# Optimization experiments

Hardware: AMD Instinct MI355X
Metric: run time of the kernel (lower is better)

Reference implementation:

```python
import jax, jax.numpy as jnp
import numpy as np

N = 100000   # num nodes
E = 1600000  # num edges (avg degree 16)
D = 32       # input_dim == latent_size
L = 3        # num_layers
K = 3        # num_hops


def setup_inputs() -> dict:
    key = jax.random.key(0)
    k0, k1, k2, k3, k4 = jax.random.split(key, 5)
    x = jax.random.normal(k0, (N, D), dtype=jnp.float32)
    edge_index = jax.random.randint(k1, (2, E), 0, N, dtype=jnp.int32)
    edge_weight = jax.random.uniform(k2, (E,), dtype=jnp.float32)
    # TAGConv per layer: K+1 bias-free Linear(in,out) weights + one bias
    W = jax.random.normal(k3, (L, K + 1, D, D), dtype=jnp.float32) * (1.0 / np.sqrt(D))
    b = jax.random.normal(k4, (L, D), dtype=jnp.float32) * 0.01
    return {"x": x, "edge_index": edge_index, "edge_weight": edge_weight, "W": W, "b": b}


def reference(x, edge_index, edge_weight, W, b):
    row, col = edge_index[0], edge_index[1]  # source, target
    # PyG gcn_norm with add_self_loops=False: deg at target, symmetric norm
    deg = jax.ops.segment_sum(edge_weight, col, num_segments=N)
    safe = jnp.where(deg > 0, deg, 1.0)
    dis = jnp.where(deg > 0, jax.lax.rsqrt(safe), 0.0)  # deg^{-1/2}
    norm = dis[row] * edge_weight * dis[col]            # [E]
    for l in range(L):
        out = x @ W[l, 0]
        h = x
        for k in range(1, K + 1):
            # one hop of normalized sparse aggregation: out[col] += norm * h[row]
            h = jax.ops.segment_sum(h[row] * norm[:, None], col, num_segments=N)
            out = out + h @ W[l, k]
        x = jax.nn.relu(out + b[l])
    return x
```

## Files before the change

### kernel.cpp

```cpp
#include <hip/hip_runtime.h>
#include <hip/hip_fp16.h>

#define NN 100000
#define NE 1600000
#define DD 32
#define NL 3
#define NK 3

#define BK 512
#define NBK ((NN + BK - 1) / BK)
#define EA 4096
#define GA ((NE + EA - 1) / EA)
#define NCNT (NBK * GA)
#define NSC ((NCNT + 255) / 256)
#define CB (NN * DD / 4 / 256)

typedef _Float16 half8 __attribute__((ext_vector_type(8)));
typedef float f32x4 __attribute__((ext_vector_type(4)));

__global__ void countA_kernel(const int* __restrict__ col, unsigned* __restrict__ cntAB,
                              const float* __restrict__ x, __half* __restrict__ xh,
                              const float* __restrict__ W, half8* __restrict__ Bpk) {
    __shared__ unsigned hc[NBK];
    int bid = blockIdx.x;
    int t = threadIdx.x;
    if (bid < GA) {
        for (int i = t; i < NBK; i += 256) hc[i] = 0;
        __syncthreads();
        int e0 = bid * EA;
        int e1 = e0 + EA; if (e1 > NE) e1 = NE;
        for (int e = e0 + t; e < e1; e += 256)
            atomicAdd(&hc[((unsigned)col[e]) >> 9], 1u);
        __syncthreads();
        for (int i = t; i < NBK; i += 256)
            cntAB[i * GA + bid] = hc[i];
    } else if (bid < GA + CB) {
        int i = (bid - GA) * 256 + t;
        f32x4 v = ((const f32x4*)x)[i];
        __half2 h01 = __floats2half2_rn(v.x, v.y);
        __half2 h23 = __floats2half2_rn(v.z, v.w);
        int2 o;
        o.x = *(int*)&h01; o.y = *(int*)&h23;
        ((int2*)xh)[i] = o;
    } else if (t < 64) {
        int l = bid - GA - CB;
        int m = t & 15, kq = t >> 4;
        for (int c = 0; c < 4; ++c) {
            for (int h = 0; h < 2; ++h) {
                half8 hi, lo;
                for (int j = 0; j < 8; ++j) {
                    float wv = W[(size_t)((l * 4 + c) * DD + kq * 8 + j) * DD + h * 16 + m];
                    _Float16 wh = (_Float16)wv;
                    hi[j] = wh;
                    lo[j] = (_Float16)(wv - (float)wh);
                }
                Bpk[(size_t)(((l * 4 + c) * 2 + h) * 2 + 0) * 64 + t] = hi;
                Bpk[(size_t)(((l * 4 + c) * 2 + h) * 2 + 1) * 64 + t] = lo;
            }
        }
    }
}

__global__ void scanb_kernel(unsigned* __restrict__ a, unsigned* __restrict__ bsum) {
    __shared__ unsigned s[256];
    int t = threadIdx.x;
    int i = blockIdx.x * 256 + t;
    unsigned v = (i < NCNT) ? a[i] : 0u;
    s[t] = v;
    __syncthreads();
    for (int off = 1; off < 256; off <<= 1) {
        unsigned add = (t >= off) ? s[t - off] : 0u;
        __syncthreads();
        s[t] += add;
        __syncthreads();
    }
    if (i < NCNT) a[i] = s[t] - v;
    if (t == 255) bsum[blockIdx.x] = s[255];
}

__global__ void scant_kernel(unsigned* __restrict__ bsum) {
    __shared__ unsigned s[512];
    int t = threadIdx.x;
    unsigned v = (t < NSC) ? bsum[t] : 0u;
    s[t] = v;
    __syncthreads();
    for (int off = 1; off < 512; off <<= 1) {
        unsigned add = (t >= off) ? s[t - off] : 0u;
        __syncthreads();
        s[t] += add;
        __syncthreads();
    }
    if (t < NSC) bsum[t] = s[t] - v;
}

__global__ void scana_kernel(unsigned* __restrict__ a, const unsigned* __restrict__ bsum,
                             unsigned* __restrict__ bbase) {
    int i = blockIdx.x * 256 + threadIdx.x;
    if (i < NCNT) {
        unsigned v = a[i] + bsum[i >> 8];
        a[i] = v;
        if (i % GA == 0) bbase[i / GA] = v;
    }
    if (i == 0) bbase[NBK] = NE;
}

__global__ void scatterC_kernel(const int* __restrict__ row, const int* __restrict__ col,
                                const float* __restrict__ w,
                                const unsigned* __restrict__ cntAB, int2* __restrict__ eb) {
    __shared__ unsigned cur[NBK];
    int bid = blockIdx.x;
    int t = threadIdx.x;
    for (int i = t; i < NBK; i += 256) cur[i] = cntAB[i * GA + bid];
    __syncthreads();
    int e0 = bid * EA;
    int e1 = e0 + EA; if (e1 > NE) e1 = NE;
    for (int e = e0 + t; e < e1; e += 256) {
        unsigned c = (unsigned)col[e];
        unsigned pos = atomicAdd(&cur[c >> 9], 1u);
        eb[pos] = make_int2((int)(((c & 511u) << 17) | (unsigned)row[e]),
                            __float_as_int(w[e]));
    }
}

__global__ void histD1_kernel(const int2* __restrict__ eb, const unsigned* __restrict__ bbase,
                              int* __restrict__ ptr, float* __restrict__ dis) {
    __shared__ unsigned h[BK];
    __shared__ unsigned ps[256];
    int b = blockIdx.x;
    int t = threadIdx.x;
    h[t] = 0; h[t + 256] = 0;
    __syncthreads();
    unsigned e0 = bbase[b], e1 = bbase[b + 1];
    for (unsigned e = e0 + t; e < e1; e += 256) {
        int2 E = eb[e];
        unsigned cl = ((unsigned)E.x) >> 17;
        float wv = __int_as_float(E.y);
        atomicAdd(&h[cl], (1u << 24) | (unsigned)(wv * 131072.0f));
    }
    __syncthreads();
    unsigned c0 = h[2 * t] >> 24, c1 = h[2 * t + 1] >> 24;
    unsigned pv = c0 + c1;
    ps[t] = pv;
    __syncthreads();
    for (int off = 1; off < 256; off <<= 1) {
        unsigned add = (t >= off) ? ps[t - off] : 0u;
        __syncthreads();
        ps[t] += add;
        __syncthreads();
    }
    unsigned base = e0 + ps[t] - pv;
    int n0 = b * BK + 2 * t;
    if (n0 < NN) {
        ptr[n0] = (int)base;
        float dg = (float)(h[2 * t] & 0xFFFFFFu) * (1.0f / 131072.0f);
        dis[n0] = dg > 0.f ? rsqrtf(dg) : 0.f;
    }
    if (n0 + 1 < NN) {
        ptr[n0 + 1] = (int)(base + c0);
        float dg = (float)(h[2 * t + 1] & 0xFFFFFFu) * (1.0f / 131072.0f);
        dis[n0 + 1] = dg > 0.f ? rsqrtf(dg) : 0.f;
    }
    if (b == 0 && t == 0) ptr[NN] = NE;
}

__global__ void fillD2_kernel(const int2* __restrict__ eb, const unsigned* __restrict__ bbase,
                              const int* __restrict__ ptr, const float* __restrict__ dis,
                              unsigned* __restrict__ epair) {
    __shared__ unsigned cur[BK];
    __shared__ float dl[BK];
    int b = blockIdx.x;
    int t = threadIdx.x;
    int n0 = b * BK;
    for (int i = t; i < BK; i += 256) {
        int n = n0 + i;
        cur[i] = (n < NN) ? (unsigned)ptr[n] : 0u;
        dl[i] = (n < NN) ? dis[n] : 0.f;
    }
    __syncthreads();
    unsigned e0 = bbase[b], e1 = bbase[b + 1];
    for (unsigned e = e0 + t; e < e1; e += 256) {
        int2 E = eb[e];
        unsigned cl = ((unsigned)E.x) >> 17;
        unsigned r = ((unsigned)E.x) & 0x1FFFFu;
        float nv = dis[r] * __int_as_float(E.y) * dl[cl];
        unsigned pos = atomicAdd(&cur[cl], 1u);
        unsigned hb = (unsigned)__half_as_ushort(__float2half(nv));
        epair[pos] = (hb << 17) | r;
    }
}

#define ACC8(rw, vv)                                                             \
    {                                                                            \
        float2 f0 = __half22float2(*reinterpret_cast<__half2*>(&rw.x));          \
        float2 f1 = __half22float2(*reinterpret_cast<__half2*>(&rw.y));          \
        float2 f2 = __half22float2(*reinterpret_cast<__half2*>(&rw.z));          \
        float2 f3 = __half22float2(*reinterpret_cast<__half2*>(&rw.w));          \
        agg[0] = fmaf(vv, f0.x, agg[0]); agg[1] = fmaf(vv, f0.y, agg[1]);        \
        agg[2] = fmaf(vv, f1.x, agg[2]); agg[3] = fmaf(vv, f1.y, agg[3]);        \
        agg[4] = fmaf(vv, f2.x, agg[4]); agg[5] = fmaf(vv, f2.y, agg[5]);        \
        agg[6] = fmaf(vv, f3.x, agg[6]); agg[7] = fmaf(vv, f3.y, agg[7]);        \
    }

__device__ __forceinline__ void gather_body16(const ushort* __restrict__ hin,
                                              const unsigned* __restrict__ epair,
                                              int p0, int p1, int st, int c4,
                                              float agg[8]) {
    const int4* hin4 = (const int4*)hin;
    int e = p0 + st;
    if (e < p1) {
        unsigned pw[8];
        int4 rw[8];
        #pragma unroll
        for (int d = 0; d < 8; ++d) {
            int ed = e + 4 * d;
            pw[d] = epair[ed < p1 ? ed : p1 - 1];
        }
        #pragma unroll
        for (int d = 0; d < 8; ++d)
            rw[d] = hin4[(size_t)(pw[d] & 0x1FFFFu) * 4 + c4];
        #pragma unroll
        for (int d = 0; d < 8; ++d) {
            float vv = (e + 4 * d < p1)
                ? __half2float(__ushort_as_half((unsigned short)(pw[d] >> 17))) : 0.f;
            ACC8(rw[d], vv);
        }
        for (e = p0 + st + 32; e < p1; e += 4) {
            unsigned p = epair[e];
            int4 r = hin4[(size_t)(p & 0x1FFFFu) * 4 + c4];
            float vv = __half2float(__ushort_as_half((unsigned short)(p >> 17)));
            ACC8(r, vv);
        }
    }
    #pragma unroll
    for (int i = 0; i < 8; ++i) {
        agg[i] += __shfl_xor(agg[i], 4, 16);
        agg[i] += __shfl_xor(agg[i], 8, 16);
    }
}

__global__ __launch_bounds__(256) void gather_kernel(
    const ushort* __restrict__ hin, ushort* __restrict__ hout,
    const int* __restrict__ ptr, const unsigned* __restrict__ epair) {
    int tid = threadIdx.x;
    int lane16 = tid & 15;
    int st = lane16 >> 2, c4 = lane16 & 3;
    int n = blockIdx.x * 16 + (tid >> 4);
    int p0 = ptr[n], p1 = ptr[n + 1];
    float agg[8] = {0.f, 0.f, 0.f, 0.f, 0.f, 0.f, 0.f, 0.f};
    gather_body16(hin, epair, p0, p1, st, c4, agg);
    if (lane16 < 4) {
        __half2 ha = __floats2half2_rn(agg[0], agg[1]);
        __half2 hb = __floats2half2_rn(agg[2], agg[3]);
        __half2 hc = __floats2half2_rn(agg[4], agg[5]);
        __half2 hd = __floats2half2_rn(agg[6], agg[7]);
        int4 pkv;
        pkv.x = *(int*)&ha; pkv.y = *(int*)&hb;
        pkv.z = *(int*)&hc; pkv.w = *(int*)&hd;
        ((int4*)hout)[(size_t)n * 4 + lane16] = pkv;
    }
}

__global__ __launch_bounds__(256) void k3ep_kernel(
    const ushort* __restrict__ f0, const ushort* __restrict__ h1,
    const ushort* __restrict__ h2,
    ushort* __restrict__ f0out, float* __restrict__ outf,
    const int* __restrict__ ptr, const unsigned* __restrict__ epair,
    const half8* __restrict__ Bp, const float* __restrict__ bias, int last) {
    __shared__ __half ldsH[16 * DD];
    int tid = threadIdx.x;
    int lane16 = tid & 15;
    int st = lane16 >> 2, c4 = lane16 & 3;
    int nloc = tid >> 4;
    int n0 = blockIdx.x * 16;
    int n = n0 + nloc;
    int p0 = ptr[n], p1 = ptr[n + 1];
    float agg[8] = {0.f, 0.f, 0.f, 0.f, 0.f, 0.f, 0.f, 0.f};
    gather_body16(h2, epair, p0, p1, st, c4, agg);
    if (lane16 < 4) {
        __half2 ha = __floats2half2_rn(agg[0], agg[1]);
        __half2 hb = __floats2half2_rn(agg[2], agg[3]);
        __half2 hc = __floats2half2_rn(agg[4], agg[5]);
        __half2 hd = __floats2half2_rn(agg[6], agg[7]);
        int4 pkv;
        pkv.x = *(int*)&ha; pkv.y = *(int*)&hb;
        pkv.z = *(int*)&hc; pkv.w = *(int*)&hd;
        *(int4*)&ldsH[nloc * DD + lane16 * 8] = pkv;
    }
    __syncthreads();
    if (tid < 64) {
        int m = tid & 15, kq = tid >> 4;
        int ai = (n0 + m) * 4 + kq;
        const half8* A0 = (const half8*)f0;
        const half8* A1 = (const half8*)h1;
        const half8* A2 = (const half8*)h2;
        f32x4 acc0 = {0.f, 0.f, 0.f, 0.f};
        f32x4 acc1 = {0.f, 0.f, 0.f, 0.f};
        half8 a;
        a = A0[ai];
        acc0 = __builtin_amdgcn_mfma_f32_16x16x32_f16(a, Bp[0 * 64 + tid], acc0, 0, 0, 0);
        acc0 = __builtin_amdgcn_mfma_f32_16x16x32_f16(a, Bp[1 * 64 + tid], acc0, 0, 0, 0);
        acc1 = __builtin_amdgcn_mfma_f32_16x16x32_f16(a, Bp[2 * 64 + tid], acc1, 0, 0, 0);
        acc1 = __builtin_amdgcn_mfma_f32_16x16x32_f16(a, Bp[3 * 64 + tid], acc1, 0, 0, 0);
        a = A1[ai];
        acc0 = __builtin_amdgcn_mfma_f32_16x16x32_f16(a, Bp[4 * 64 + tid], acc0, 0, 0, 0);
        acc0 = __builtin_amdgcn_mfma_f32_16x16x32_f16(a, Bp[5 * 64 + tid], acc0, 0, 0, 0);
        acc1 = __builtin_amdgcn_mfma_f32_16x16x32_f16(a, Bp[6 * 64 + tid], acc1, 0, 0, 0);
        acc1 = __builtin_amdgcn_mfma_f32_16x16x32_f16(a, Bp[7 * 64 + tid], acc1, 0, 0, 0);
        a = A2[ai];
        acc0 = __builtin_amdgcn_mfma_f32_16x16x32_f16(a, Bp[8 * 64 + tid], acc0, 0, 0, 0);
        acc0 = __builtin_amdgcn_mfma_f32_16x16x32_f16(a, Bp[9 * 64 + tid], acc0, 0, 0, 0);
        acc1 = __builtin_amdgcn_mfma_f32_16x16x32_f16(a, Bp[10 * 64 + tid], acc1, 0, 0, 0);
        acc1 = __builtin_amdgcn_mfma_f32_16x16x32_f16(a, Bp[11 * 64 + tid], acc1, 0, 0, 0);
        a = *(const half8*)&ldsH[m * DD + kq * 8];
        acc0 = __builtin_amdgcn_mfma_f32_16x16x32_f16(a, Bp[12 * 64 + tid], acc0, 0, 0, 0);
        acc0 = __builtin_amdgcn_mfma_f32_16x16x32_f16(a, Bp[13 * 64 + tid], acc0, 0, 0, 0);
        acc1 = __builtin_amdgcn_mfma_f32_16x16x32_f16(a, Bp[14 * 64 + tid], acc1, 0, 0, 0);
        acc1 = __builtin_amdgcn_mfma_f32_16x16x32_f16(a, Bp[15 * 64 + tid], acc1, 0, 0, 0);
        float b0 = bias[m], b1 = bias[16 + m];
        #pragma unroll
        for (int r = 0; r < 4; ++r) {
            int rowi = n0 + kq * 4 + r;
            float v0 = fmaxf(acc0[r] + b0, 0.f);
            float v1 = fmaxf(acc1[r] + b1, 0.f);
            if (last) {
                outf[rowi * DD + m] = v0;
                outf[rowi * DD + 16 + m] = v1;
            } else {
                ((__half*)f0out)[rowi * DD + m] = __float2half(v0);
                ((__half*)f0out)[rowi * DD + 16 + m] = __float2half(v1);
            }
        }
    }
}

extern "C" void kernel_launch(void* const* d_in, const int* in_sizes, int n_in,
                              void* d_out, int out_size, void* d_ws, size_t ws_size,
                              hipStream_t stream) {
    const float* x  = (const float*)d_in[0];
    const int*   ei = (const int*)d_in[1];
    const float* ew = (const float*)d_in[2];
    const float* W  = (const float*)d_in[3];
    const float* b  = (const float*)d_in[4];
    float* out = (float*)d_out;

    const int* row = ei;
    const int* col = ei + NE;

    char* base = (char*)d_ws;
    int2*     eb    = (int2*)base;
    ushort*   h1    = (ushort*)base;
    ushort*   h2    = (ushort*)(base + 6400000);
    unsigned* epair = (unsigned*)(base + 12800000);
    ushort*   f0    = (ushort*)(base + 19200000);
    int*      ptr   = (int*)(base + 25600000);
    float*    dis   = (float*)(base + 26000016);
    unsigned* cntAB = (unsigned*)(base + 26400016);
    unsigned* bsum  = (unsigned*)(base + 26706560);
    unsigned* bbase = (unsigned*)(base + 26707776);
    half8*    Bpk   = (half8*)(base + 26708576);

    countA_kernel<<<GA + CB + NL, 256, 0, stream>>>(col, cntAB, x, (__half*)f0, W, Bpk);
    scanb_kernel<<<NSC, 256, 0, stream>>>(cntAB, bsum);
    scant_kernel<<<1, 512, 0, stream>>>(bsum);
    scana_kernel<<<NSC, 256, 0, stream>>>(cntAB, bsum, bbase);
    scatterC_kernel<<<GA, 256, 0, stream>>>(row, col, ew, cntAB, eb);
    histD1_kernel<<<NBK, 256, 0, stream>>>(eb, bbase, ptr, dis);
    fillD2_kernel<<<NBK, 256, 0, stream>>>(eb, bbase, ptr, dis, epair);

    const int grid = NN / 16;
    for (int l = 0; l < NL; ++l) {
        int lastl = (l == NL - 1);
        gather_kernel<<<grid, 256, 0, stream>>>(f0, h1, ptr, epair);
        gather_kernel<<<grid, 256, 0, stream>>>(h1, h2, ptr, epair);
        k3ep_kernel<<<grid, 256, 0, stream>>>(f0, h1, h2, f0, out, ptr, epair,
                                              Bpk + (size_t)l * 1024,
                                              b + (size_t)l * DD, lastl);
    }
}
```

Before: 315.0 us.

## Split feature matrices into lo/hi column planes and use persistent gather grids

Node features are stored as two 16-column half planes instead of one 32-column row, and each gather pass processes one plane at a time. The likely aim is to halve the working set per pass so random neighbor reads hit cache more often. The gather and fused epilogue kernels become persistent grid-stride loops over 1024 blocks with occupancy hints, and edge-list loads and stores are marked nontemporal. In exchange, epair and ptr are read twice per hop, and the fused kernel keeps several tiles in LDS with a per-tile barrier.

Result: slower. 442.7 us (+40.5%).

```diff
diff --git a/kernel.cpp b/kernel.cpp
--- a/kernel.cpp
+++ b/kernel.cpp
@@ -15,11 +15,17 @@
 #define NSC ((NCNT + 255) / 256)
 #define CB (NN * DD / 4 / 256)
 
+#define GRID 1024
+#define NG (NN / 16)
+#define GMAX 7
+
 typedef _Float16 half8 __attribute__((ext_vector_type(8)));
 typedef float f32x4 __attribute__((ext_vector_type(4)));
+typedef int i32x4 __attribute__((ext_vector_type(4)));
 
 __global__ void countA_kernel(const int* __restrict__ col, unsigned* __restrict__ cntAB,
-                              const float* __restrict__ x, __half* __restrict__ xh,
+                              const float* __restrict__ x,
+                              __half* __restrict__ xlo, __half* __restrict__ xhi,
                               const float* __restrict__ W, half8* __restrict__ Bpk) {
     __shared__ unsigned hc[NBK];
     int bid = blockIdx.x;
@@ -41,7 +47,9 @@
         __half2 h23 = __floats2half2_rn(v.z, v.w);
         int2 o;
         o.x = *(int*)&h01; o.y = *(int*)&h23;
-        ((int2*)xh)[i] = o;
+        int n = i >> 3, j = i & 7;
+        __half* dst = (j < 4) ? xlo : xhi;
+        ((int2*)dst)[n * 4 + (j & 3)] = o;
     } else if (t < 64) {
         int l = bid - GA - CB;
         int m = t & 15, kq = t >> 4;
@@ -201,133 +209,174 @@
         agg[6] = fmaf(vv, f3.x, agg[6]); agg[7] = fmaf(vv, f3.y, agg[7]);        \
     }
 
-__device__ __forceinline__ void gather_body16(const ushort* __restrict__ hin,
-                                              const unsigned* __restrict__ epair,
-                                              int p0, int p1, int st, int c4,
-                                              float agg[8]) {
-    const int4* hin4 = (const int4*)hin;
+__device__ __forceinline__ void gseg(const ushort* __restrict__ pin,
+                                     const unsigned* __restrict__ epair,
+                                     int p0, int p1, int st, int c2,
+                                     float agg[8]) {
+    const int4* pin4 = (const int4*)pin;
     int e = p0 + st;
     if (e < p1) {
-        unsigned pw[8];
-        int4 rw[8];
+        unsigned pw[4];
+        int4 rw[4];
         #pragma unroll
-        for (int d = 0; d < 8; ++d) {
-            int ed = e + 4 * d;
-            pw[d] = epair[ed < p1 ? ed : p1 - 1];
+        for (int d = 0; d < 4; ++d) {
+            int ed = e + 8 * d;
+            pw[d] = __builtin_nontemporal_load(epair + (ed < p1 ? ed : p1 - 1));
         }
         #pragma unroll
-        for (int d = 0; d < 8; ++d)
-            rw[d] = hin4[(size_t)(pw[d] & 0x1FFFFu) * 4 + c4];
+        for (int d = 0; d < 4; ++d)
+            rw[d] = pin4[(size_t)(pw[d] & 0x1FFFFu) * 2 + c2];
         #pragma unroll
-        for (int d = 0; d < 8; ++d) {
-            float vv = (e + 4 * d < p1)
+        for (int d = 0; d < 4; ++d) {
+            float vv = (e + 8 * d < p1)
                 ? __half2float(__ushort_as_half((unsigned short)(pw[d] >> 17))) : 0.f;
             ACC8(rw[d], vv);
         }
-        for (e = p0 + st + 32; e < p1; e += 4) {
-            unsigned p = epair[e];
-            int4 r = hin4[(size_t)(p & 0x1FFFFu) * 4 + c4];
+        for (e = p0 + st + 32; e < p1; e += 8) {
+            unsigned p = __builtin_nontemporal_load(epair + e);
+            int4 r = pin4[(size_t)(p & 0x1FFFFu) * 2 + c2];
             float vv = __half2float(__ushort_as_half((unsigned short)(p >> 17)));
             ACC8(r, vv);
         }
     }
     #pragma unroll
     for (int i = 0; i < 8; ++i) {
+        agg[i] += __shfl_xor(agg[i], 2, 16);
         agg[i] += __shfl_xor(agg[i], 4, 16);
         agg[i] += __shfl_xor(agg[i], 8, 16);
     }
 }
 
-__global__ __launch_bounds__(256) void gather_kernel(
-    const ushort* __restrict__ hin, ushort* __restrict__ hout,
+__device__ __forceinline__ void hop_plane(const ushort* __restrict__ pin,
+                                          ushort* __restrict__ pout,
+                                          const int* __restrict__ ptr,
+                                          const unsigned* __restrict__ epair,
+                                          int tid, int bid) {
+    int lane16 = tid & 15;
+    int st = lane16 >> 1, c2 = lane16 & 1;
+    int nl = tid >> 4;
+    for (int g = bid; g < NG; g += GRID) {
+        int n = g * 16 + nl;
+        int p0 = ptr[n], p1 = ptr[n + 1];
+        float agg[8] = {0.f, 0.f, 0.f, 0.f, 0.f, 0.f, 0.f, 0.f};
+        gseg(pin, epair, p0, p1, st, c2, agg);
+        if (lane16 < 2) {
+            __half2 ha = __floats2half2_rn(agg[0], agg[1]);
+            __half2 hb = __floats2half2_rn(agg[2], agg[3]);
+            __half2 hc = __floats2half2_rn(agg[4], agg[5]);
+            __half2 hd = __floats2half2_rn(agg[6], agg[7]);
+            i32x4 pkv;
+            pkv[0] = *(int*)&ha; pkv[1] = *(int*)&hb;
+            pkv[2] = *(int*)&hc; pkv[3] = *(int*)&hd;
+            __builtin_nontemporal_store(pkv, (i32x4*)pout + (size_t)n * 2 + c2);
+        }
+    }
+}
+
+__global__ __launch_bounds__(256, 4) void gather_kernel(
+    const ushort* __restrict__ pin_lo, const ushort* __restrict__ pin_hi,
+    ushort* __restrict__ pout_lo, ushort* __restrict__ pout_hi,
     const int* __restrict__ ptr, const unsigned* __restrict__ epair) {
     int tid = threadIdx.x;
-    int lane16 = tid & 15;
-    int st = lane16 >> 2, c4 = lane16 & 3;
-    int n = blockIdx.x * 16 + (tid >> 4);
-    int p0 = ptr[n], p1 = ptr[n + 1];
-    float agg[8] = {0.f, 0.f, 0.f, 0.f, 0.f, 0.f, 0.f, 0.f};
-    gather_body16(hin, epair, p0, p1, st, c4, agg);
-    if (lane16 < 4) {
-        __half2 ha = __floats2half2_rn(agg[0], agg[1]);
-        __half2 hb = __floats2half2_rn(agg[2], agg[3]);
-        __half2 hc = __floats2half2_rn(agg[4], agg[5]);
-        __half2 hd = __floats2half2_rn(agg[6], agg[7]);
-        int4 pkv;
-        pkv.x = *(int*)&ha; pkv.y = *(int*)&hb;
-        pkv.z = *(int*)&hc; pkv.w = *(int*)&hd;
-        ((int4*)hout)[(size_t)n * 4 + lane16] = pkv;
-    }
-}
-
-__global__ __launch_bounds__(256) void k3ep_kernel(
-    const ushort* __restrict__ f0, const ushort* __restrict__ h1,
-    const ushort* __restrict__ h2,
-    ushort* __restrict__ f0out, float* __restrict__ outf,
+    int bid = blockIdx.x;
+    hop_plane(pin_lo, pout_lo, ptr, epair, tid, bid);
+    hop_plane(pin_hi, pout_hi, ptr, epair, tid, bid);
+}
+
+__global__ __launch_bounds__(256, 4) void k3ep_kernel(
+    const ushort* __restrict__ f0lo, const ushort* __restrict__ f0hi,
+    const ushort* __restrict__ h1lo, const ushort* __restrict__ h1hi,
+    const ushort* __restrict__ h2lo, const ushort* __restrict__ h2hi,
+    ushort* __restrict__ f0outlo, ushort* __restrict__ f0outhi,
+    float* __restrict__ outf,
     const int* __restrict__ ptr, const unsigned* __restrict__ epair,
     const half8* __restrict__ Bp, const float* __restrict__ bias, int last) {
-    __shared__ __half ldsH[16 * DD];
+    __shared__ __align__(16) __half ldsT[GMAX][16 * DD];
     int tid = threadIdx.x;
+    int bid = blockIdx.x;
     int lane16 = tid & 15;
-    int st = lane16 >> 2, c4 = lane16 & 3;
-    int nloc = tid >> 4;
-    int n0 = blockIdx.x * 16;
-    int n = n0 + nloc;
-    int p0 = ptr[n], p1 = ptr[n + 1];
-    float agg[8] = {0.f, 0.f, 0.f, 0.f, 0.f, 0.f, 0.f, 0.f};
-    gather_body16(h2, epair, p0, p1, st, c4, agg);
-    if (lane16 < 4) {
-        __half2 ha = __floats2half2_rn(agg[0], agg[1]);
-        __half2 hb = __floats2half2_rn(agg[2], agg[3]);
-        __half2 hc = __floats2half2_rn(agg[4], agg[5]);
-        __half2 hd = __floats2half2_rn(agg[6], agg[7]);
-        int4 pkv;
-        pkv.x = *(int*)&ha; pkv.y = *(int*)&hb;
-        pkv.z = *(int*)&hc; pkv.w = *(int*)&hd;
-        *(int4*)&ldsH[nloc * DD + lane16 * 8] = pkv;
-    }
-    __syncthreads();
-    if (tid < 64) {
-        int m = tid & 15, kq = tid >> 4;
-        int ai = (n0 + m) * 4 + kq;
-        const half8* A0 = (const half8*)f0;
-        const half8* A1 = (const half8*)h1;
-        const half8* A2 = (const half8*)h2;
-        f32x4 acc0 = {0.f, 0.f, 0.f, 0.f};
-        f32x4 acc1 = {0.f, 0.f, 0.f, 0.f};
-        half8 a;
-        a = A0[ai];
-        acc0 = __builtin_amdgcn_mfma_f32_16x16x32_f16(a, Bp[0 * 64 + tid], acc0, 0, 0, 0);
-        acc0 = __builtin_amdgcn_mfma_f32_16x16x32_f16(a, Bp[1 * 64 + tid], acc0, 0, 0, 0);
-        acc1 = __builtin_amdgcn_mfma_f32_16x16x32_f16(a, Bp[2 * 64 + tid], acc1, 0, 0, 0);
-        acc1 = __builtin_amdgcn_mfma_f32_16x16x32_f16(a, Bp[3 * 64 + tid], acc1, 0, 0, 0);
-        a = A1[ai];
-        acc0 = __builtin_amdgcn_mfma_f32_16x16x32_f16(a, Bp[4 * 64 + tid], acc0, 0, 0, 0);
-        acc0 = __builtin_amdgcn_mfma_f32_16x16x32_f16(a, Bp[5 * 64 + tid], acc0, 0, 0, 0);
-        acc1 = __builtin_amdgcn_mfma_f32_16x16x32_f16(a, Bp[6 * 64 + tid], acc1, 0, 0, 0);
-        acc1 = __builtin_amdgcn_mfma_f32_16x16x32_f16(a, Bp[7 * 64 + tid], acc1, 0, 0, 0);
-        a = A2[ai];
-        acc0 = __builtin_amdgcn_mfma_f32_16x16x32_f16(a, Bp[8 * 64 + tid], acc0, 0, 0, 0);
-        acc0 = __builtin_amdgcn_mfma_f32_16x16x32_f16(a, Bp[9 * 64 + tid], acc0, 0, 0, 0);
-        acc1 = __builtin_amdgcn_mfma_f32_16x16x32_f16(a, Bp[10 * 64 + tid], acc1, 0, 0, 0);
-        acc1 = __builtin_amdgcn_mfma_f32_16x16x32_f16(a, Bp[11 * 64 + tid], acc1, 0, 0, 0);
-        a = *(const half8*)&ldsH[m * DD + kq * 8];
-        acc0 = __builtin_amdgcn_mfma_f32_16x16x32_f16(a, Bp[12 * 64 + tid], acc0, 0, 0, 0);
-        acc0 = __builtin_amdgcn_mfma_f32_16x16x32_f16(a, Bp[13 * 64 + tid], acc0, 0, 0, 0);
-        acc1 = __builtin_amdgcn_mfma_f32_16x16x32_f16(a, Bp[14 * 64 + tid], acc1, 0, 0, 0);
-        acc1 = __builtin_amdgcn_mfma_f32_16x16x32_f16(a, Bp[15 * 64 + tid], acc1, 0, 0, 0);
-        float b0 = bias[m], b1 = bias[16 + m];
-        #pragma unroll
-        for (int r = 0; r < 4; ++r) {
-            int rowi = n0 + kq * 4 + r;
-            float v0 = fmaxf(acc0[r] + b0, 0.f);
-            float v1 = fmaxf(acc1[r] + b1, 0.f);
-            if (last) {
-                outf[rowi * DD + m] = v0;
-                outf[rowi * DD + 16 + m] = v1;
-            } else {
-                ((__half*)f0out)[rowi * DD + m] = __float2half(v0);
-                ((__half*)f0out)[rowi * DD + 16 + m] = __float2half(v1);
+    int st = lane16 >> 1, c2 = lane16 & 1;
+    int nl = tid >> 4;
+    {
+        int k = 0;
+        for (int g = bid; g < NG; g += GRID, ++k) {
+            int n = g * 16 + nl;
+            int p0 = ptr[n], p1 = ptr[n + 1];
+            float agg[8] = {0.f, 0.f, 0.f, 0.f, 0.f, 0.f, 0.f, 0.f};
+            gseg(h2lo, epair, p0, p1, st, c2, agg);
+            if (lane16 < 2) {
+                __half2 ha = __floats2half2_rn(agg[0], agg[1]);
+                __half2 hb = __floats2half2_rn(agg[2], agg[3]);
+                __half2 hc = __floats2half2_rn(agg[4], agg[5]);
+                __half2 hd = __floats2half2_rn(agg[6], agg[7]);
+                int4 pkv;
+                pkv.x = *(int*)&ha; pkv.y = *(int*)&hb;
+                pkv.z = *(int*)&hc; pkv.w = *(int*)&hd;
+                *(int4*)&ldsT[k][nl * DD + c2 * 8] = pkv;
+            }
+        }
+    }
+    {
+        int k = 0;
+        for (int g = bid; g < NG; g += GRID, ++k) {
+            int n = g * 16 + nl;
+            int p0 = ptr[n], p1 = ptr[n + 1];
+            float agg[8] = {0.f, 0.f, 0.f, 0.f, 0.f, 0.f, 0.f, 0.f};
+            gseg(h2hi, epair, p0, p1, st, c2, agg);
+            if (lane16 < 2) {
+                __half2 ha = __floats2half2_rn(agg[0], agg[1]);
+                __half2 hb = __floats2half2_rn(agg[2], agg[3]);
+                __half2 hc = __floats2half2_rn(agg[4], agg[5]);
+                __half2 hd = __floats2half2_rn(agg[6], agg[7]);
+                int4 pkv;
+                pkv.x = *(int*)&ha; pkv.y = *(int*)&hb;
+                pkv.z = *(int*)&hc; pkv.w = *(int*)&hd;
+                *(int4*)&ldsT[k][nl * DD + 16 + c2 * 8] = pkv;
+            }
+            __syncthreads();
+            if (tid < 64) {
+                int m = tid & 15, kq = tid >> 4;
+                int ai = (g * 16 + m) * 2 + (kq & 1);
+                const half8* A0 = (kq < 2) ? (const half8*)f0lo : (const half8*)f0hi;
+                const half8* A1 = (kq < 2) ? (const half8*)h1lo : (const half8*)h1hi;
+                const half8* A2 = (kq < 2) ? (const half8*)h2lo : (const half8*)h2hi;
+                f32x4 acc0 = {0.f, 0.f, 0.f, 0.f};
+                f32x4 acc1 = {0.f, 0.f, 0.f, 0.f};
+                half8 a;
+                a = A0[ai];
+                acc0 = __builtin_amdgcn_mfma_f32_16x16x32_f16(a, Bp[0 * 64 + tid], acc0, 0, 0, 0);
+                acc0 = __builtin_amdgcn_mfma_f32_16x16x32_f16(a, Bp[1 * 64 + tid], acc0, 0, 0, 0);
+                acc1 = __builtin_amdgcn_mfma_f32_16x16x32_f16(a, Bp[2 * 64 + tid], acc1, 0, 0, 0);
+                acc1 = __builtin_amdgcn_mfma_f32_16x16x32_f16(a, Bp[3 * 64 + tid], acc1, 0, 0, 0);
+                a = A1[ai];
+                acc0 = __builtin_amdgcn_mfma_f32_16x16x32_f16(a, Bp[4 * 64 + tid], acc0, 0, 0, 0);
+                acc0 = __builtin_amdgcn_mfma_f32_16x16x32_f16(a, Bp[5 * 64 + tid], acc0, 0, 0, 0);
+                acc1 = __builtin_amdgcn_mfma_f32_16x16x32_f16(a, Bp[6 * 64 + tid], acc1, 0, 0, 0);
+                acc1 = __builtin_amdgcn_mfma_f32_16x16x32_f16(a, Bp[7 * 64 + tid], acc1, 0, 0, 0);
+                a = A2[ai];
+                acc0 = __builtin_amdgcn_mfma_f32_16x16x32_f16(a, Bp[8 * 64 + tid], acc0, 0, 0, 0);
+                acc0 = __builtin_amdgcn_mfma_f32_16x16x32_f16(a, Bp[9 * 64 + tid], acc0, 0, 0, 0);
+                acc1 = __builtin_amdgcn_mfma_f32_16x16x32_f16(a, Bp[10 * 64 + tid], acc1, 0, 0, 0);
+                acc1 = __builtin_amdgcn_mfma_f32_16x16x32_f16(a, Bp[11 * 64 + tid], acc1, 0, 0, 0);
+                a = *(const half8*)&ldsT[k][m * DD + kq * 8];
+                acc0 = __builtin_amdgcn_mfma_f32_16x16x32_f16(a, Bp[12 * 64 + tid], acc0, 0, 0, 0);
+                acc0 = __builtin_amdgcn_mfma_f32_16x16x32_f16(a, Bp[13 * 64 + tid], acc0, 0, 0, 0);
+                acc1 = __builtin_amdgcn_mfma_f32_16x16x32_f16(a, Bp[14 * 64 + tid], acc1, 0, 0, 0);
+                acc1 = __builtin_amdgcn_mfma_f32_16x16x32_f16(a, Bp[15 * 64 + tid], acc1, 0, 0, 0);
+                float b0 = bias[m], b1 = bias[16 + m];
+                #pragma unroll
+                for (int r = 0; r < 4; ++r) {
+                    int rowi = g * 16 + kq * 4 + r;
+                    float v0 = fmaxf(acc0[r] + b0, 0.f);
+                    float v1 = fmaxf(acc1[r] + b1, 0.f);
+                    if (last) {
+                        outf[rowi * DD + m] = v0;
+                        outf[rowi * DD + 16 + m] = v1;
+                    } else {
+                        ((__half*)f0outlo)[rowi * 16 + m] = __float2half(v0);
+                        ((__half*)f0outhi)[rowi * 16 + m] = __float2half(v1);
+                    }
+                }
             }
         }
     }
@@ -348,10 +397,13 @@
 
     char* base = (char*)d_ws;
     int2*     eb    = (int2*)base;
-    ushort*   h1    = (ushort*)base;
-    ushort*   h2    = (ushort*)(base + 6400000);
+    ushort*   h1lo  = (ushort*)base;
+    ushort*   h1hi  = (ushort*)(base + 3200000);
+    ushort*   h2lo  = (ushort*)(base + 6400000);
+    ushort*   h2hi  = (ushort*)(base + 9600000);
     unsigned* epair = (unsigned*)(base + 12800000);
-    ushort*   f0    = (ushort*)(base + 19200000);
+    ushort*   f0lo  = (ushort*)(base + 19200000);
+    ushort*   f0hi  = (ushort*)(base + 22400000);
     int*      ptr   = (int*)(base + 25600000);
     float*    dis   = (float*)(base + 26000016);
     unsigned* cntAB = (unsigned*)(base + 26400016);
@@ -359,7 +411,8 @@
     unsigned* bbase = (unsigned*)(base + 26707776);
     half8*    Bpk   = (half8*)(base + 26708576);
 
-    countA_kernel<<<GA + CB + NL, 256, 0, stream>>>(col, cntAB, x, (__half*)f0, W, Bpk);
+    countA_kernel<<<GA + CB + NL, 256, 0, stream>>>(col, cntAB, x,
+                                                    (__half*)f0lo, (__half*)f0hi, W, Bpk);
     scanb_kernel<<<NSC, 256, 0, stream>>>(cntAB, bsum);
     scant_kernel<<<1, 512, 0, stream>>>(bsum);
     scana_kernel<<<NSC, 256, 0, stream>>>(cntAB, bsum, bbase);
@@ -367,12 +420,12 @@
     histD1_kernel<<<NBK, 256, 0, stream>>>(eb, bbase, ptr, dis);
     fillD2_kernel<<<NBK, 256, 0, stream>>>(eb, bbase, ptr, dis, epair);
 
-    const int grid = NN / 16;
     for (int l = 0; l < NL; ++l) {
         int lastl = (l == NL - 1);
-        gather_kernel<<<grid, 256, 0, stream>>>(f0, h1, ptr, epair);
-        gather_kernel<<<grid, 256, 0, stream>>>(h1, h2, ptr, epair);
-        k3ep_kernel<<<grid, 256, 0, stream>>>(f0, h1, h2, f0, out, ptr, epair,
+        gather_kernel<<<GRID, 256, 0, stream>>>(f0lo, f0hi, h1lo, h1hi, ptr, epair);
+        gather_kernel<<<GRID, 256, 0, stream>>>(h1lo, h1hi, h2lo, h2hi, ptr, epair);
+        k3ep_kernel<<<GRID, 256, 0, stream>>>(f0lo, f0hi, h1lo, h1hi, h2lo, h2hi,
+                                              f0lo, f0hi, out, ptr, epair,
                                               Bpk + (size_t)l * 1024,
                                               b + (size_t)l * DD, lastl);
     }
```

## Fuse per-layer hop and epilogue kernels into persistent kernel with grid barriers

Applied to the files above, without the earlier changes.

Replaces the two gather launches and the k3ep launch per layer with one persistent layer_kernel of 1024 blocks. Each block loops over node groups, and the phases are separated by a software grid barrier built on agent-scope atomics. The goal is to cut kernel launch and drain/fill overhead between dependent hops. In exchange, correctness depends on all 1024 blocks being co-resident, since the launch is not cooperative. The fixed grid and barrier spinning may also lower parallelism and latency hiding.

Measured after the change: 1.116 ms. 3.54x slower.

```diff
diff --git a/kernel.cpp b/kernel.cpp
--- a/kernel.cpp
+++ b/kernel.cpp
@@ -14,6 +14,9 @@
 #define NCNT (NBK * GA)
 #define NSC ((NCNT + 255) / 256)
 #define CB (NN * DD / 4 / 256)
+
+#define GRID 1024
+#define NG (NN / 16)
 
 typedef _Float16 half8 __attribute__((ext_vector_type(8)));
 typedef float f32x4 __attribute__((ext_vector_type(4)));
@@ -189,6 +192,24 @@
     }
 }
 
+__device__ __forceinline__ void gridbar(unsigned* bar) {
+    __syncthreads();
+    if (threadIdx.x == 0) {
+        __threadfence();
+        unsigned g = __hip_atomic_load(bar + 1, __ATOMIC_RELAXED, __HIP_MEMORY_SCOPE_AGENT);
+        unsigned old = __hip_atomic_fetch_add(bar, 1u, __ATOMIC_RELAXED, __HIP_MEMORY_SCOPE_AGENT);
+        if (old == GRID - 1) {
+            __hip_atomic_fetch_sub(bar, (unsigned)GRID, __ATOMIC_RELAXED, __HIP_MEMORY_SCOPE_AGENT);
+            __hip_atomic_fetch_add(bar + 1, 1u, __ATOMIC_RELAXED, __HIP_MEMORY_SCOPE_AGENT);
+        } else {
+            while (__hip_atomic_load(bar + 1, __ATOMIC_RELAXED, __HIP_MEMORY_SCOPE_AGENT) == g)
+                __builtin_amdgcn_s_sleep(1);
+        }
+        __threadfence();
+    }
+    __syncthreads();
+}
+
 #define ACC8(rw, vv)                                                             \
     {                                                                            \
         float2 f0 = __half22float2(*reinterpret_cast<__half2*>(&rw.x));          \
@@ -238,13 +259,11 @@
     }
 }
 
-__global__ __launch_bounds__(256) void gather_kernel(
-    const ushort* __restrict__ hin, ushort* __restrict__ hout,
-    const int* __restrict__ ptr, const unsigned* __restrict__ epair) {
-    int tid = threadIdx.x;
-    int lane16 = tid & 15;
-    int st = lane16 >> 2, c4 = lane16 & 3;
-    int n = blockIdx.x * 16 + (tid >> 4);
+__device__ __forceinline__ void hop_group(const ushort* __restrict__ hin,
+                                          ushort* __restrict__ hout,
+                                          const int* __restrict__ ptr,
+                                          const unsigned* __restrict__ epair,
+                                          int n, int lane16, int st, int c4) {
     int p0 = ptr[n], p1 = ptr[n + 1];
     float agg[8] = {0.f, 0.f, 0.f, 0.f, 0.f, 0.f, 0.f, 0.f};
     gather_body16(hin, epair, p0, p1, st, c4, agg);
@@ -260,76 +279,87 @@
     }
 }
 
-__global__ __launch_bounds__(256) void k3ep_kernel(
-    const ushort* __restrict__ f0, const ushort* __restrict__ h1,
-    const ushort* __restrict__ h2,
-    ushort* __restrict__ f0out, float* __restrict__ outf,
+__global__ __launch_bounds__(256, 4) void layer_kernel(
+    ushort* __restrict__ f0, ushort* __restrict__ h1, ushort* __restrict__ h2,
+    float* __restrict__ outf,
     const int* __restrict__ ptr, const unsigned* __restrict__ epair,
-    const half8* __restrict__ Bp, const float* __restrict__ bias, int last) {
+    const half8* __restrict__ Bp, const float* __restrict__ bias, int last,
+    unsigned* __restrict__ bar) {
     __shared__ __half ldsH[16 * DD];
     int tid = threadIdx.x;
+    int bid = blockIdx.x;
     int lane16 = tid & 15;
     int st = lane16 >> 2, c4 = lane16 & 3;
-    int nloc = tid >> 4;
-    int n0 = blockIdx.x * 16;
-    int n = n0 + nloc;
-    int p0 = ptr[n], p1 = ptr[n + 1];
-    float agg[8] = {0.f, 0.f, 0.f, 0.f, 0.f, 0.f, 0.f, 0.f};
-    gather_body16(h2, epair, p0, p1, st, c4, agg);
-    if (lane16 < 4) {
-        __half2 ha = __floats2half2_rn(agg[0], agg[1]);
-        __half2 hb = __floats2half2_rn(agg[2], agg[3]);
-        __half2 hc = __floats2half2_rn(agg[4], agg[5]);
-        __half2 hd = __floats2half2_rn(agg[6], agg[7]);
-        int4 pkv;
-        pkv.x = *(int*)&ha; pkv.y = *(int*)&hb;
-        pkv.z = *(int*)&hc; pkv.w = *(int*)&hd;
-        *(int4*)&ldsH[nloc * DD + lane16 * 8] = pkv;
-    }
-    __syncthreads();
-    if (tid < 64) {
-        int m = tid & 15, kq = tid >> 4;
-        int ai = (n0 + m) * 4 + kq;
-        const half8* A0 = (const half8*)f0;
-        const half8* A1 = (const half8*)h1;
-        const half8* A2 = (const half8*)h2;
-        f32x4 acc0 = {0.f, 0.f, 0.f, 0.f};
-        f32x4 acc1 = {0.f, 0.f, 0.f, 0.f};
-        half8 a;
-        a = A0[ai];
-        acc0 = __builtin_amdgcn_mfma_f32_16x16x32_f16(a, Bp[0 * 64 + tid], acc0, 0, 0, 0);
-        acc0 = __builtin_amdgcn_mfma_f32_16x16x32_f16(a, Bp[1 * 64 + tid], acc0, 0, 0, 0);
-        acc1 = __builtin_amdgcn_mfma_f32_16x16x32_f16(a, Bp[2 * 64 + tid], acc1, 0, 0, 0);
-        acc1 = __builtin_amdgcn_mfma_f32_16x16x32_f16(a, Bp[3 * 64 + tid], acc1, 0, 0, 0);
-        a = A1[ai];
-        acc0 = __builtin_amdgcn_mfma_f32_16x16x32_f16(a, Bp[4 * 64 + tid], acc0, 0, 0, 0);
-        acc0 = __builtin_amdgcn_mfma_f32_16x16x32_f16(a, Bp[5 * 64 + tid], acc0, 0, 0, 0);
-        acc1 = __builtin_amdgcn_mfma_f32_16x16x32_f16(a, Bp[6 * 64 + tid], acc1, 0, 0, 0);
-        acc1 = __builtin_amdgcn_mfma_f32_16x16x32_f16(a, Bp[7 * 64 + tid], acc1, 0, 0, 0);
-        a = A2[ai];
-        acc0 = __builtin_amdgcn_mfma_f32_16x16x32_f16(a, Bp[8 * 64 + tid], acc0, 0, 0, 0);
-        acc0 = __builtin_amdgcn_mfma_f32_16x16x32_f16(a, Bp[9 * 64 + tid], acc0, 0, 0, 0);
-        acc1 = __builtin_amdgcn_mfma_f32_16x16x32_f16(a, Bp[10 * 64 + tid], acc1, 0, 0, 0);
-        acc1 = __builtin_amdgcn_mfma_f32_16x16x32_f16(a, Bp[11 * 64 + tid], acc1, 0, 0, 0);
-        a = *(const half8*)&ldsH[m * DD + kq * 8];
-        acc0 = __builtin_amdgcn_mfma_f32_16x16x32_f16(a, Bp[12 * 64 + tid], acc0, 0, 0, 0);
-        acc0 = __builtin_amdgcn_mfma_f32_16x16x32_f16(a, Bp[13 * 64 + tid], acc0, 0, 0, 0);
-        acc1 = __builtin_amdgcn_mfma_f32_16x16x32_f16(a, Bp[14 * 64 + tid], acc1, 0, 0, 0);
-        acc1 = __builtin_amdgcn_mfma_f32_16x16x32_f16(a, Bp[15 * 64 + tid], acc1, 0, 0, 0);
-        float b0 = bias[m], b1 = bias[16 + m];
-        #pragma unroll
-        for (int r = 0; r < 4; ++r) {
-            int rowi = n0 + kq * 4 + r;
-            float v0 = fmaxf(acc0[r] + b0, 0.f);
-            float v1 = fmaxf(acc1[r] + b1, 0.f);
-            if (last) {
-                outf[rowi * DD + m] = v0;
-                outf[rowi * DD + 16 + m] = v1;
-            } else {
-                ((__half*)f0out)[rowi * DD + m] = __float2half(v0);
-                ((__half*)f0out)[rowi * DD + 16 + m] = __float2half(v1);
+    int nl = tid >> 4;
+
+    for (int g = bid; g < NG; g += GRID)
+        hop_group(f0, h1, ptr, epair, g * 16 + nl, lane16, st, c4);
+    gridbar(bar);
+    for (int g = bid; g < NG; g += GRID)
+        hop_group(h1, h2, ptr, epair, g * 16 + nl, lane16, st, c4);
+    gridbar(bar);
+    for (int g = bid; g < NG; g += GRID) {
+        int n0 = g * 16;
+        int n = n0 + nl;
+        int p0 = ptr[n], p1 = ptr[n + 1];
+        float agg[8] = {0.f, 0.f, 0.f, 0.f, 0.f, 0.f, 0.f, 0.f};
+        gather_body16(h2, epair, p0, p1, st, c4, agg);
+        if (lane16 < 4) {
+            __half2 ha = __floats2half2_rn(agg[0], agg[1]);
+            __half2 hb = __floats2half2_rn(agg[2], agg[3]);
+            __half2 hc = __floats2half2_rn(agg[4], agg[5]);
+            __half2 hd = __floats2half2_rn(agg[6], agg[7]);
+            int4 pkv;
+            pkv.x = *(int*)&ha; pkv.y = *(int*)&hb;
+            pkv.z = *(int*)&hc; pkv.w = *(int*)&hd;
+            *(int4*)&ldsH[nl * DD + lane16 * 8] = pkv;
+        }
+        __syncthreads();
+        if (tid < 64) {
+            int m = tid & 15, kq = tid >> 4;
+            int ai = (n0 + m) * 4 + kq;
+            const half8* A0 = (const half8*)f0;
+            const half8* A1 = (const half8*)h1;
+            const half8* A2 = (const half8*)h2;
+            f32x4 acc0 = {0.f, 0.f, 0.f, 0.f};
+            f32x4 acc1 = {0.f, 0.f, 0.f, 0.f};
+            half8 a;
+            a = A0[ai];
+            acc0 = __builtin_amdgcn_mfma_f32_16x16x32_f16(a, Bp[0 * 64 + tid], acc0, 0, 0, 0);
+            acc0 = __builtin_amdgcn_mfma_f32_16x16x32_f16(a, Bp[1 * 64 + tid], acc0, 0, 0, 0);
+            acc1 = __builtin_amdgcn_mfma_f32_16x16x32_f16(a, Bp[2 * 64 + tid], acc1, 0, 0, 0);
+            acc1 = __builtin_amdgcn_mfma_f32_16x16x32_f16(a, Bp[3 * 64 + tid], acc1, 0, 0, 0);
+            a = A1[ai];
+            acc0 = __builtin_amdgcn_mfma_f32_16x16x32_f16(a, Bp[4 * 64 + tid], acc0, 0, 0, 0);
+            acc0 = __builtin_amdgcn_mfma_f32_16x16x32_f16(a, Bp[5 * 64 + tid], acc0, 0, 0, 0);
+            acc1 = __builtin_amdgcn_mfma_f32_16x16x32_f16(a, Bp[6 * 64 + tid], acc1, 0, 0, 0);
+            acc1 = __builtin_amdgcn_mfma_f32_16x16x32_f16(a, Bp[7 * 64 + tid], acc1, 0, 0, 0);
+            a = A2[ai];
+            acc0 = __builtin_amdgcn_mfma_f32_16x16x32_f16(a, Bp[8 * 64 + tid], acc0, 0, 0, 0);
+            acc0 = __builtin_amdgcn_mfma_f32_16x16x32_f16(a, Bp[9 * 64 + tid], acc0, 0, 0, 0);
+            acc1 = __builtin_amdgcn_mfma_f32_16x16x32_f16(a, Bp[10 * 64 + tid], acc1, 0, 0, 0);
+            acc1 = __builtin_amdgcn_mfma_f32_16x16x32_f16(a, Bp[11 * 64 + tid], acc1, 0, 0, 0);
+            a = *(const half8*)&ldsH[m * DD + kq * 8];
+            acc0 = __builtin_amdgcn_mfma_f32_16x16x32_f16(a, Bp[12 * 64 + tid], acc0, 0, 0, 0);
+            acc0 = __builtin_amdgcn_mfma_f32_16x16x32_f16(a, Bp[13 * 64 + tid], acc0, 0, 0, 0);
+            acc1 = __builtin_amdgcn_mfma_f32_16x16x32_f16(a, Bp[14 * 64 + tid], acc1, 0, 0, 0);
+            acc1 = __builtin_amdgcn_mfma_f32_16x16x32_f16(a, Bp[15 * 64 + tid], acc1, 0, 0, 0);
+            float b0 = bias[m], b1 = bias[16 + m];
+            #pragma unroll
+            for (int r = 0; r < 4; ++r) {
+                int rowi = n0 + kq * 4 + r;
+                float v0 = fmaxf(acc0[r] + b0, 0.f);
+                float v1 = fmaxf(acc1[r] + b1, 0.f);
+                if (last) {
+                    outf[rowi * DD + m] = v0;
+                    outf[rowi * DD + 16 + m] = v1;
+                } else {
+                    ((__half*)f0)[rowi * DD + m] = __float2half(v0);
+                    ((__half*)f0)[rowi * DD + 16 + m] = __float2half(v1);
+                }
             }
         }
+        __syncthreads();
     }
 }
 
@@ -358,7 +388,9 @@
     unsigned* bsum  = (unsigned*)(base + 26706560);
     unsigned* bbase = (unsigned*)(base + 26707776);
     half8*    Bpk   = (half8*)(base + 26708576);
-
+    unsigned* bar   = (unsigned*)(base + 26757728);
+
+    hipMemsetAsync(bar, 0, 2 * sizeof(unsigned), stream);
     countA_kernel<<<GA + CB + NL, 256, 0, stream>>>(col, cntAB, x, (__half*)f0, W, Bpk);
     scanb_kernel<<<NSC, 256, 0, stream>>>(cntAB, bsum);
     scant_kernel<<<1, 512, 0, stream>>>(bsum);
@@ -367,13 +399,10 @@
     histD1_kernel<<<NBK, 256, 0, stream>>>(eb, bbase, ptr, dis);
     fillD2_kernel<<<NBK, 256, 0, stream>>>(eb, bbase, ptr, dis, epair);
 
-    const int grid = NN / 16;
     for (int l = 0; l < NL; ++l) {
         int lastl = (l == NL - 1);
-        gather_kernel<<<grid, 256, 0, stream>>>(f0, h1, ptr, epair);
-        gather_kernel<<<grid, 256, 0, stream>>>(h1, h2, ptr, epair);
-        k3ep_kernel<<<grid, 256, 0, stream>>>(f0, h1, h2, f0, out, ptr, epair,
-                                              Bpk + (size_t)l * 1024,
-                                              b + (size_t)l * DD, lastl);
-    }
-}
+        layer_kernel<<<GRID, 256, 0, stream>>>(f0, h1, h2, out, ptr, epair,
+                                               Bpk + (size_t)l * 1024,
+                                               b + (size_t)l * DD, lastl, bar);
+    }
+}
```
